# Optimization experiments

Hardware: AMD Instinct MI355X
Metric: run time of the kernel (lower is better)

The kernel has to match this reference:

```python
import jax, jax.numpy as jnp
import numpy as np

B, S, D, H = 32, 2048, 1024, 1024

def setup_inputs() -> dict:
    key = jax.random.key(0)
    k1, k2, k3, k4, k5 = jax.random.split(key, 5)
    return {
        "query": jax.random.normal(k1, (B, D), dtype=jnp.float32),
        "values": jax.random.normal(k2, (B, S, D), dtype=jnp.float32),
        "W1": jax.random.normal(k3, (D, H), dtype=jnp.float32) / np.sqrt(D),
        "W2": jax.random.normal(k4, (D, H), dtype=jnp.float32) / np.sqrt(D),
        "v": jax.random.uniform(k5, (H,), dtype=jnp.float32),
    }

def reference(query, values, W1, W2, v):
    # query: [B, D], values: [B, S, D]
    query_proj = query @ W2                              # [B, H]
    keys_proj = jnp.einsum('bsd,dh->bsh', values, W1)     # [B, S, H]
    energy = jnp.tanh(query_proj[:, None, :] + keys_proj) # [B, S, H]
    scores = jnp.einsum('bsh,h->bs', energy, v)           # [B, S]
    attention_weights = jax.nn.softmax(scores, axis=-1)   # [B, S]
    context = jnp.einsum('bs,bsd->bd', attention_weights, values)  # [B, D]
    return context, attention_weights
```

## Files before the change

### kernel.cpp

```cpp
#include <hip/hip_runtime.h>
#include <hip/hip_fp16.h>


typedef _Float16 v8h  __attribute__((ext_vector_type(8)));
typedef __fp16   v2hf __attribute__((ext_vector_type(2)));
typedef float    v4f  __attribute__((ext_vector_type(4)));

#define B_DIM 32
#define S_DIM 2048
#define D_DIM 1024
#define H_DIM 1024

#define WS_W1T    0u
#define WS_QP     2097152u
#define WS_SCORES (WS_QP + 131072u)

__device__ __forceinline__ void gl_lds16(const _Float16* g, _Float16* l) {
    __builtin_amdgcn_global_load_lds(
        (const __attribute__((address_space(1))) void*)g,
        (__attribute__((address_space(3))) void*)l, 16, 0, 0);
}

__global__ void k_prep(const float* __restrict__ W1, _Float16* __restrict__ w1t,
                       const float* __restrict__ query, const float* __restrict__ W2,
                       float* __restrict__ qp, float* __restrict__ scores) {
    __shared__ float smem[64 * 65];
    int bid = blockIdx.x, tid = threadIdx.x;
    if (bid < 256) {
        int b = bid >> 3, hc = bid & 7;
        #pragma unroll
        for (int i = 0; i < 4; ++i)
            smem[i * 256 + tid] = query[b * D_DIM + i * 256 + tid];
        __syncthreads();
        int hh = tid & 127, half = tid >> 7;
        int h = hc * 128 + hh;
        const float* w2p = W2 + (size_t)(half * 512) * H_DIM + h;
        float acc = 0.f;
        #pragma unroll 8
        for (int d = 0; d < 512; ++d)
            acc += smem[half * 512 + d] * w2p[(size_t)d * H_DIM];
        smem[1024 + tid] = acc;
        __syncthreads();
        if (tid < 128)
            qp[b * H_DIM + hc * 128 + tid] = smem[1024 + tid] + smem[1024 + 128 + tid];
    } else if (bid < 512) {
        int j = bid - 256;
        int h0 = (j & 15) * 64, d0 = (j >> 4) * 64;
        #pragma unroll
        for (int i = 0; i < 16; ++i) {
            int idx = i * 256 + tid;
            int dd = idx >> 6, hh = idx & 63;
            smem[dd * 65 + hh] = W1[(size_t)(d0 + dd) * H_DIM + h0 + hh];
        }
        __syncthreads();
        #pragma unroll
        for (int i = 0; i < 16; ++i) {
            int idx = i * 256 + tid;
            int hh = idx >> 6, dd = idx & 63;
            w1t[(size_t)(h0 + hh) * D_DIM + d0 + dd] = (_Float16)smem[dd * 65 + hh];
        }
    } else {
        int j = bid - 512;
        size_t o = (size_t)j * 2048 + tid * 8;
        *(v4f*)(scores + o)     = (v4f){0.f, 0.f, 0.f, 0.f};
        *(v4f*)(scores + o + 4) = (v4f){0.f, 0.f, 0.f, 0.f};
    }
}

__global__ __launch_bounds__(512, 2) void k_scores(
        const float* __restrict__ values, const _Float16* __restrict__ w1t,
        const float* __restrict__ qp, const float* __restrict__ v,
        float* __restrict__ scores) {
    __shared__ _Float16 As[256 * 64];
    __shared__ _Float16 Bs[256 * 64];

    int tid = threadIdx.x;
    int wid = tid >> 6, lane = tid & 63;
    int quad = lane >> 4, l15 = lane & 15;
    int wm = wid >> 2, wn = wid & 3;

    int bid = blockIdx.x;
    int idx = (bid & 7) * 128 + (bid >> 3);
    int np  = idx & 3;
    int mtb = idx >> 2;
    int b   = mtb >> 3;
    int m0  = (mtb & 7) * 256;
    int n0  = np * 256;

    int arow  = tid >> 3;
    int aslot = tid & 7;
    const float* abase = values + ((size_t)b * S_DIM + m0) * D_DIM;
    int a_row[4], a_off[4];
    #pragma unroll
    for (int i = 0; i < 4; ++i) {
        int row  = i * 64 + arow;
        a_row[i] = row;
        a_off[i] = row * 64 + (aslot ^ (row & 7)) * 8;
    }

    int srow = lane >> 3;
    int kg   = lane & 7;

    v4f acc[8][4];
    #pragma unroll
    for (int i = 0; i < 8; ++i)
        #pragma unroll
        for (int j = 0; j < 4; ++j) acc[i][j] = (v4f){0.f, 0.f, 0.f, 0.f};

    v4f ap[8];
    #pragma unroll
    for (int i = 0; i < 4; ++i) {
        const float* p = abase + (size_t)a_row[i] * D_DIM + aslot * 8;
        ap[2 * i]     = *(const v4f*)p;
        ap[2 * i + 1] = *(const v4f*)(p + 4);
    }
    #pragma unroll
    for (int i = 0; i < 4; ++i) {
        int brow = i * 64 + wid * 8;
        int row  = brow + srow;
        int kgs  = kg ^ (row & 7);
        gl_lds16(w1t + (size_t)(n0 + row) * D_DIM + kgs * 8, &Bs[brow * 64]);
    }
    #pragma unroll
    for (int i = 0; i < 4; ++i) {
        union { v8h h; v2hf p[4]; } u;
        u.p[0] = __builtin_amdgcn_cvt_pkrtz(ap[2 * i][0], ap[2 * i][1]);
        u.p[1] = __builtin_amdgcn_cvt_pkrtz(ap[2 * i][2], ap[2 * i][3]);
        u.p[2] = __builtin_amdgcn_cvt_pkrtz(ap[2 * i + 1][0], ap[2 * i + 1][1]);
        u.p[3] = __builtin_amdgcn_cvt_pkrtz(ap[2 * i + 1][2], ap[2 * i + 1][3]);
        *(v8h*)(&As[a_off[i]]) = u.h;
    }
    __syncthreads();

    for (int kt = 0; kt < 16; ++kt) {
        int k1 = ((kt + 1) & 15) * 64;
        #pragma unroll
        for (int i = 0; i < 4; ++i) {
            const float* p = abase + (size_t)a_row[i] * D_DIM + k1 + aslot * 8;
            ap[2 * i]     = *(const v4f*)p;
            ap[2 * i + 1] = *(const v4f*)(p + 4);
        }
        __builtin_amdgcn_sched_barrier(0);

        #pragma unroll
        for (int kk = 0; kk < 2; ++kk) {
            v8h af[8], bf[4];
            #pragma unroll
            for (int mt = 0; mt < 8; ++mt) {
                int row = wm * 128 + mt * 16 + l15;
                int ph  = (kk * 4 + quad) ^ (row & 7);
                af[mt] = *(const v8h*)(&As[row * 64 + ph * 8]);
            }
            #pragma unroll
            for (int nt = 0; nt < 4; ++nt) {
                int row = wn * 64 + nt * 16 + l15;
                int ph  = (kk * 4 + quad) ^ (row & 7);
                bf[nt] = *(const v8h*)(&Bs[row * 64 + ph * 8]);
            }
            #pragma unroll
            for (int mt = 0; mt < 8; ++mt)
                #pragma unroll
                for (int nt = 0; nt < 4; ++nt)
                    acc[mt][nt] = __builtin_amdgcn_mfma_f32_16x16x32_f16(
                        af[mt], bf[nt], acc[mt][nt], 0, 0, 0);
        }
        __syncthreads();

        if (kt < 15) {
            #pragma unroll
            for (int i = 0; i < 4; ++i) {
                int brow = i * 64 + wid * 8;
                int row  = brow + srow;
                int kgs  = kg ^ (row & 7);
                gl_lds16(w1t + (size_t)(n0 + row) * D_DIM + k1 + kgs * 8, &Bs[brow * 64]);
            }
            #pragma unroll
            for (int i = 0; i < 4; ++i) {
                union { v8h h; v2hf p[4]; } u;
                u.p[0] = __builtin_amdgcn_cvt_pkrtz(ap[2 * i][0], ap[2 * i][1]);
                u.p[1] = __builtin_amdgcn_cvt_pkrtz(ap[2 * i][2], ap[2 * i][3]);
                u.p[2] = __builtin_amdgcn_cvt_pkrtz(ap[2 * i + 1][0], ap[2 * i + 1][1]);
                u.p[3] = __builtin_amdgcn_cvt_pkrtz(ap[2 * i + 1][2], ap[2 * i + 1][3]);
                *(v8h*)(&As[a_off[i]]) = u.h;
            }
        }
        __syncthreads();
    }

    float qpv[4], vv[4];
    #pragma unroll
    for (int nt = 0; nt < 4; ++nt) {
        int ng = n0 + wn * 64 + nt * 16 + l15;
        qpv[nt] = qp[b * H_DIM + ng];
        vv[nt]  = v[ng];
    }

    float* s_scores = (float*)As;
    if (tid < 256) s_scores[tid] = 0.f;
    __syncthreads();

    #pragma unroll
    for (int mt = 0; mt < 8; ++mt) {
        #pragma unroll
        for (int r = 0; r < 4; ++r) {
            float s = 0.f;
            #pragma unroll
            for (int nt = 0; nt < 4; ++nt) {
                float x = acc[mt][nt][r] + qpv[nt];
                float e = __expf(2.f * x);
                s += (1.f - 2.f / (e + 1.f)) * vv[nt];
            }
            s += __shfl_xor(s, 1);
            s += __shfl_xor(s, 2);
            s += __shfl_xor(s, 4);
            s += __shfl_xor(s, 8);
            if (l15 == 0)
                atomicAdd(&s_scores[wm * 128 + mt * 16 + quad * 4 + r], s);
        }
    }
    __syncthreads();
    if (tid < 256) atomicAdd(&scores[(size_t)b * S_DIM + m0 + tid], s_scores[tid]);
}

__global__ __launch_bounds__(1024) void k_finish(
        const float* __restrict__ scores, const float* __restrict__ values,
        float* __restrict__ wout, float* __restrict__ ctx) {
    __shared__ float s_w[2048];
    __shared__ int   s_idx[2048];
    __shared__ float red[16];
    __shared__ float s_bcast;
    __shared__ int   s_cnt;

    int b = blockIdx.x, tid = threadIdx.x;
    int lane = tid & 63, wid = tid >> 6;

    float s0 = scores[b * S_DIM + tid];
    float s1 = scores[b * S_DIM + 1024 + tid];

    float m = fmaxf(s0, s1);
    #pragma unroll
    for (int off = 1; off <= 32; off <<= 1) m = fmaxf(m, __shfl_xor(m, off));
    if (lane == 0) red[wid] = m;
    if (tid == 0) s_cnt = 0;
    __syncthreads();
    if (tid == 0) {
        float mm = red[0];
        #pragma unroll
        for (int i = 1; i < 16; ++i) mm = fmaxf(mm, red[i]);
        s_bcast = mm;
    }
    __syncthreads();
    float rowmax = s_bcast;

    float e0 = __expf(s0 - rowmax);
    float e1 = __expf(s1 - rowmax);
    float sum = e0 + e1;
    #pragma unroll
    for (int off = 1; off <= 32; off <<= 1) sum += __shfl_xor(sum, off);
    if (lane == 0) red[wid] = sum;
    __syncthreads();
    if (tid == 0) {
        float ss = red[0];
        #pragma unroll
        for (int i = 1; i < 16; ++i) ss += red[i];
        s_bcast = 1.f / ss;
    }
    __syncthreads();
    float inv = s_bcast;

    float w0 = e0 * inv, w1 = e1 * inv;
    wout[b * S_DIM + tid]        = w0;
    wout[b * S_DIM + 1024 + tid] = w1;
    s_w[tid]        = w0;
    s_w[tid + 1024] = w1;

    if (w0 > 1e-7f) { int p = atomicAdd(&s_cnt, 1); s_idx[p] = tid; }
    if (w1 > 1e-7f) { int p = atomicAdd(&s_cnt, 1); s_idx[p] = tid + 1024; }
    __syncthreads();
    int cnt = s_cnt;

    float acc = 0.f;
    const float* vb = values + (size_t)b * S_DIM * D_DIM + tid;
    for (int i = 0; i < cnt; ++i) {
        int s = s_idx[i];
        acc += s_w[s] * vb[(size_t)s * D_DIM];
    }
    ctx[b * D_DIM + tid] = acc;
}

extern "C" void kernel_launch(void* const* d_in, const int* in_sizes, int n_in,
                              void* d_out, int out_size, void* d_ws, size_t ws_size,
                              hipStream_t stream) {
    const float* query  = (const float*)d_in[0];
    const float* values = (const float*)d_in[1];
    const float* W1     = (const float*)d_in[2];
    const float* W2     = (const float*)d_in[3];
    const float* v      = (const float*)d_in[4];

    char* ws = (char*)d_ws;
    _Float16* w1t = (_Float16*)(ws + WS_W1T);
    float* qp     = (float*)(ws + WS_QP);
    float* scores = (float*)(ws + WS_SCORES);

    float* ctx  = (float*)d_out;
    float* wout = (float*)d_out + 32768;

    k_prep<<<dim3(544), 256, 0, stream>>>(W1, w1t, query, W2, qp, scores);
    k_scores<<<dim3(1024), 512, 0, stream>>>(values, w1t, qp, v, scores);
    k_finish<<<dim3(32), 1024, 0, stream>>>(scores, values, wout, ctx);
}
```

Measured before the change: 569.6 us.

## Double-buffer LDS tiles in scores GEMM with single barrier per k-step

Splits the A and B shared-memory tiles into two buffers so the next k-tile is converted and staged into one buffer while MFMAs read the other. Global loads of values are prefetched two steps ahead, and the two __syncthreads per iteration become one explicit waitcnt plus barrier. MFMA sections are wrapped in s_setprio to favour compute waves. LDS per block doubles to 128KB, which likely no longer allows the two blocks per CU that the launch bounds ask for, so occupancy may drop.

Result: slower. 591.6 us (+3.9%).

```diff
diff --git a/kernel.cpp b/kernel.cpp
--- a/kernel.cpp
+++ b/kernel.cpp
@@ -71,8 +71,8 @@
         const float* __restrict__ values, const _Float16* __restrict__ w1t,
         const float* __restrict__ qp, const float* __restrict__ v,
         float* __restrict__ scores) {
-    __shared__ _Float16 As[256 * 64];
-    __shared__ _Float16 Bs[256 * 64];
+    __shared__ _Float16 As[2][256 * 64];
+    __shared__ _Float16 Bs[2][256 * 64];
 
     int tid = threadIdx.x;
     int wid = tid >> 6, lane = tid & 63;
@@ -108,18 +108,12 @@
         for (int j = 0; j < 4; ++j) acc[i][j] = (v4f){0.f, 0.f, 0.f, 0.f};
 
     v4f ap[8];
+
     #pragma unroll
     for (int i = 0; i < 4; ++i) {
         const float* p = abase + (size_t)a_row[i] * D_DIM + aslot * 8;
         ap[2 * i]     = *(const v4f*)p;
         ap[2 * i + 1] = *(const v4f*)(p + 4);
-    }
-    #pragma unroll
-    for (int i = 0; i < 4; ++i) {
-        int brow = i * 64 + wid * 8;
-        int row  = brow + srow;
-        int kgs  = kg ^ (row & 7);
-        gl_lds16(w1t + (size_t)(n0 + row) * D_DIM + kgs * 8, &Bs[brow * 64]);
     }
     #pragma unroll
     for (int i = 0; i < 4; ++i) {
@@ -128,52 +122,27 @@
         u.p[1] = __builtin_amdgcn_cvt_pkrtz(ap[2 * i][2], ap[2 * i][3]);
         u.p[2] = __builtin_amdgcn_cvt_pkrtz(ap[2 * i + 1][0], ap[2 * i + 1][1]);
         u.p[3] = __builtin_amdgcn_cvt_pkrtz(ap[2 * i + 1][2], ap[2 * i + 1][3]);
-        *(v8h*)(&As[a_off[i]]) = u.h;
-    }
-    __syncthreads();
+        *(v8h*)(&As[0][a_off[i]]) = u.h;
+    }
+    #pragma unroll
+    for (int i = 0; i < 4; ++i) {
+        int brow = i * 64 + wid * 8;
+        int row  = brow + srow;
+        int kgs  = kg ^ (row & 7);
+        gl_lds16(w1t + (size_t)(n0 + row) * D_DIM + kgs * 8, &Bs[0][brow * 64]);
+    }
+    #pragma unroll
+    for (int i = 0; i < 4; ++i) {
+        const float* p = abase + (size_t)a_row[i] * D_DIM + 64 + aslot * 8;
+        ap[2 * i]     = *(const v4f*)p;
+        ap[2 * i + 1] = *(const v4f*)(p + 4);
+    }
+    asm volatile("s_waitcnt vmcnt(8) lgkmcnt(0)" ::: "memory");
+    __builtin_amdgcn_s_barrier();
 
     for (int kt = 0; kt < 16; ++kt) {
-        int k1 = ((kt + 1) & 15) * 64;
-        #pragma unroll
-        for (int i = 0; i < 4; ++i) {
-            const float* p = abase + (size_t)a_row[i] * D_DIM + k1 + aslot * 8;
-            ap[2 * i]     = *(const v4f*)p;
-            ap[2 * i + 1] = *(const v4f*)(p + 4);
-        }
-        __builtin_amdgcn_sched_barrier(0);
-
-        #pragma unroll
-        for (int kk = 0; kk < 2; ++kk) {
-            v8h af[8], bf[4];
-            #pragma unroll
-            for (int mt = 0; mt < 8; ++mt) {
-                int row = wm * 128 + mt * 16 + l15;
-                int ph  = (kk * 4 + quad) ^ (row & 7);
-                af[mt] = *(const v8h*)(&As[row * 64 + ph * 8]);
-            }
-            #pragma unroll
-            for (int nt = 0; nt < 4; ++nt) {
-                int row = wn * 64 + nt * 16 + l15;
-                int ph  = (kk * 4 + quad) ^ (row & 7);
-                bf[nt] = *(const v8h*)(&Bs[row * 64 + ph * 8]);
-            }
-            #pragma unroll
-            for (int mt = 0; mt < 8; ++mt)
-                #pragma unroll
-                for (int nt = 0; nt < 4; ++nt)
-                    acc[mt][nt] = __builtin_amdgcn_mfma_f32_16x16x32_f16(
-                        af[mt], bf[nt], acc[mt][nt], 0, 0, 0);
-        }
-        __syncthreads();
-
+        int cur = kt & 1;
         if (kt < 15) {
-            #pragma unroll
-            for (int i = 0; i < 4; ++i) {
-                int brow = i * 64 + wid * 8;
-                int row  = brow + srow;
-                int kgs  = kg ^ (row & 7);
-                gl_lds16(w1t + (size_t)(n0 + row) * D_DIM + k1 + kgs * 8, &Bs[brow * 64]);
-            }
             #pragma unroll
             for (int i = 0; i < 4; ++i) {
                 union { v8h h; v2hf p[4]; } u;
@@ -181,10 +150,54 @@
                 u.p[1] = __builtin_amdgcn_cvt_pkrtz(ap[2 * i][2], ap[2 * i][3]);
                 u.p[2] = __builtin_amdgcn_cvt_pkrtz(ap[2 * i + 1][0], ap[2 * i + 1][1]);
                 u.p[3] = __builtin_amdgcn_cvt_pkrtz(ap[2 * i + 1][2], ap[2 * i + 1][3]);
-                *(v8h*)(&As[a_off[i]]) = u.h;
-            }
-        }
-        __syncthreads();
+                *(v8h*)(&As[cur ^ 1][a_off[i]]) = u.h;
+            }
+            int k1 = (kt + 1) * 64;
+            #pragma unroll
+            for (int i = 0; i < 4; ++i) {
+                int brow = i * 64 + wid * 8;
+                int row  = brow + srow;
+                int kgs  = kg ^ (row & 7);
+                gl_lds16(w1t + (size_t)(n0 + row) * D_DIM + k1 + kgs * 8,
+                         &Bs[cur ^ 1][brow * 64]);
+            }
+            int k2 = ((kt + 2) & 15) * 64;
+            #pragma unroll
+            for (int i = 0; i < 4; ++i) {
+                const float* p = abase + (size_t)a_row[i] * D_DIM + k2 + aslot * 8;
+                ap[2 * i]     = *(const v4f*)p;
+                ap[2 * i + 1] = *(const v4f*)(p + 4);
+            }
+            __builtin_amdgcn_sched_barrier(0);
+        }
+
+        __builtin_amdgcn_s_setprio(1);
+        #pragma unroll
+        for (int kk = 0; kk < 2; ++kk) {
+            v8h af[8], bf[4];
+            #pragma unroll
+            for (int mt = 0; mt < 8; ++mt) {
+                int row = wm * 128 + mt * 16 + l15;
+                int ph  = (kk * 4 + quad) ^ (row & 7);
+                af[mt] = *(const v8h*)(&As[cur][row * 64 + ph * 8]);
+            }
+            #pragma unroll
+            for (int nt = 0; nt < 4; ++nt) {
+                int row = wn * 64 + nt * 16 + l15;
+                int ph  = (kk * 4 + quad) ^ (row & 7);
+                bf[nt] = *(const v8h*)(&Bs[cur][row * 64 + ph * 8]);
+            }
+            #pragma unroll
+            for (int mt = 0; mt < 8; ++mt)
+                #pragma unroll
+                for (int nt = 0; nt < 4; ++nt)
+                    acc[mt][nt] = __builtin_amdgcn_mfma_f32_16x16x32_f16(
+                        af[mt], bf[nt], acc[mt][nt], 0, 0, 0);
+        }
+        __builtin_amdgcn_s_setprio(0);
+
+        asm volatile("s_waitcnt vmcnt(8) lgkmcnt(0)" ::: "memory");
+        __builtin_amdgcn_s_barrier();
     }
 
     float qpv[4], vv[4];
@@ -195,7 +208,7 @@
         vv[nt]  = v[ng];
     }
 
-    float* s_scores = (float*)As;
+    float* s_scores = (float*)&As[0][0];
     if (tid < 256) s_scores[tid] = 0.f;
     __syncthreads();
 
```
